# Kernel optimization log

Hardware: AMD Instinct MI355X
Metric: run time of the kernel (lower is better)

Reference implementation:

```python
import jax, jax.numpy as jnp
import numpy as np

B, T, D, H = 2, 2048, 1024, 16
HD = D // H            # 64
FH = 2752              # SwiGLU hidden: round64(int(2*4*D/3))
BETA_INIT = 0.5


def rmsnorm(x, w, eps=1e-6):
    x32 = x.astype(jnp.float32)
    r = jax.lax.rsqrt(jnp.mean(x32 * x32, axis=-1, keepdims=True) + eps)
    return (x32 * r).astype(x.dtype) * w


def rope(x, cos, sin):
    # x: (B,H,T,HD); cos/sin: (T,HD//2)
    d2 = x.shape[-1] // 2
    x1, x2 = x[..., :d2], x[..., d2:]
    return jnp.concatenate([x1 * cos - x2 * sin, x2 * cos + x1 * sin], axis=-1)


def delta_res(x, h, gn_w, g_w, g_b, wv_w, eps_k=1e-6):
    # k-hat = normalize(h); k = k_hat / sqrt(d)
    h32 = h.astype(jnp.float32)
    nrm = jnp.sqrt(jnp.sum(h32 * h32, axis=-1, keepdims=True))
    k = (h32 / jnp.maximum(nrm, eps_k)).astype(x.dtype) * (1.0 / np.sqrt(D))
    c = rmsnorm(x, gn_w)
    logit = c @ g_w + g_b                                   # (B,T)
    beta = (2.0 * jax.nn.sigmoid(logit.astype(jnp.float32))).astype(x.dtype)[..., None]
    v = jax.nn.sigmoid(x @ wv_w)[..., None]                 # (B,T,1)
    kTx = jnp.sum(k * x, axis=-1, keepdims=True)
    return x + beta * (v - kTx) * k


def setup_inputs() -> dict:
    key = jax.random.key(0)
    ks = jax.random.split(key, 12)
    s = 0.02
    gb = np.float32(np.log(BETA_INIT / 2.0 / (1.0 - BETA_INIT / 2.0 + 1e-8)))
    return {
        "x": jax.random.normal(ks[0], (B, T, D), jnp.float32),
        "wq": jax.random.normal(ks[1], (D, D), jnp.float32) * s,
        "wk": jax.random.normal(ks[2], (D, D), jnp.float32) * s,
        "wv": jax.random.normal(ks[3], (D, D), jnp.float32) * s,
        "wo": jax.random.normal(ks[4], (D, D), jnp.float32) * s,
        "qn_w": jnp.ones((HD,), jnp.float32),
        "kn_w": jnp.ones((HD,), jnp.float32),
        "attn_norm_w": jnp.ones((D,), jnp.float32),
        "g1_norm_w": jnp.ones((D,), jnp.float32),
        "g1_w": jax.random.normal(ks[5], (D,), jnp.float32) * s,
        "g1_b": jnp.asarray(gb),
        "wv1": jax.random.normal(ks[6], (D,), jnp.float32) * s,
        "mlp_norm_w": jnp.ones((D,), jnp.float32),
        "w1": jax.random.normal(ks[7], (FH, D), jnp.float32) * s,
        "w2": jax.random.normal(ks[8], (D, FH), jnp.float32) * s,
        "w3": jax.random.normal(ks[9], (FH, D), jnp.float32) * s,
        "g2_norm_w": jnp.ones((D,), jnp.float32),
        "g2_w": jax.random.normal(ks[10], (D,), jnp.float32) * s,
        "g2_b": jnp.asarray(gb),
        "wv2": jax.random.normal(ks[11], (D,), jnp.float32) * s,
    }


def reference(x, wq, wk, wv, wo, qn_w, kn_w, attn_norm_w,
              g1_norm_w, g1_w, g1_b, wv1, mlp_norm_w, w1, w2, w3,
              g2_norm_w, g2_w, g2_b, wv2):
    # ---- attention sublayer (pre-norm) ----
    xc = rmsnorm(x, attn_norm_w)
    q = (xc @ wq.T).reshape(B, T, H, HD).swapaxes(1, 2)   # (B,H,T,HD)
    k = (xc @ wk.T).reshape(B, T, H, HD).swapaxes(1, 2)
    v = (xc @ wv.T).reshape(B, T, H, HD).swapaxes(1, 2)
    q = rmsnorm(q, qn_w)
    k = rmsnorm(k, kn_w)
    inv_freq = 1.0 / (10000.0 ** (jnp.arange(0, HD, 2, dtype=jnp.float32) / HD))
    freqs = jnp.arange(T, dtype=jnp.float32)[:, None] * inv_freq[None, :]  # (T,HD/2)
    cos, sin = jnp.cos(freqs), jnp.sin(freqs)
    q = rope(q, cos, sin)
    k = rope(k, cos, sin)
    scale = 1.0 / np.sqrt(HD)
    scores = jnp.einsum('bhqd,bhkd->bhqk', q, k) * scale
    causal = jnp.where(jnp.arange(T)[:, None] >= jnp.arange(T)[None, :], 0.0, -jnp.inf).astype(scores.dtype)
    attn = jax.nn.softmax(scores + causal, axis=-1)
    out = jnp.einsum('bhqk,bhkd->bhqd', attn, v)
    h_attn = out.swapaxes(1, 2).reshape(B, T, D) @ wo.T
    x = delta_res(x, h_attn, g1_norm_w, g1_w, g1_b, wv1)
    # ---- MLP sublayer (pre-norm SwiGLU) ----
    xm = rmsnorm(x, mlp_norm_w)
    h_mlp = (jax.nn.silu(xm @ w1.T) * (xm @ w3.T)) @ w2.T
    x = delta_res(x, h_mlp, g2_norm_w, g2_w, g2_b, wv2)
    return x
```

## Files before the change

### kernel.cpp

```cpp
#include <hip/hip_runtime.h>
#include <hip/hip_bf16.h>
#include <math.h>

using bf16 = __hip_bfloat16;
typedef __bf16 bf16x8 __attribute__((ext_vector_type(8)));
typedef float f32x4 __attribute__((ext_vector_type(4)));

static constexpr int B_ = 2, T_ = 2048, D_ = 1024, H_ = 16, HD_ = 64, FH_ = 2752;
static constexpr int BT = B_ * T_;

struct __align__(8)  bh4 { bf16 h[4]; };
struct __align__(16) bh8 { bf16 h[8]; };

#define DEV static __device__ __forceinline__

DEV float b2f(bf16 v) { return __bfloat162float(v); }
DEV bf16  f2b(float v) { return __float2bfloat16(v); }
DEV __bf16 f2bb(float f) { __hip_bfloat16 h = __float2bfloat16(f); return *reinterpret_cast<__bf16*>(&h); }
DEV float sigmoidf_(float x) { return 1.0f / (1.0f + __expf(-x)); }

DEV void load4f(const bf16* p, float* v) {
    bh4 t = *reinterpret_cast<const bh4*>(p);
#pragma unroll
    for (int i = 0; i < 4; ++i) v[i] = b2f(t.h[i]);
}
DEV void load4f(const float* p, float* v) {
    float4 t = *reinterpret_cast<const float4*>(p);
    v[0] = t.x; v[1] = t.y; v[2] = t.z; v[3] = t.w;
}
DEV void store4(float* p, const float* v) {
    float4 t; t.x = v[0]; t.y = v[1]; t.z = v[2]; t.w = v[3];
    *reinterpret_cast<float4*>(p) = t;
}
DEV float waveReduceSum(float v) {
#pragma unroll
    for (int m = 32; m; m >>= 1) v += __shfl_xor(v, m);
    return v;
}

DEV void gl_lds16(const bf16* g, bf16* lds_base) {
    __builtin_amdgcn_global_load_lds(
        (const __attribute__((address_space(1))) void*)g,
        (__attribute__((address_space(3))) void*)lds_base, 16, 0, 0);
}

__global__ __launch_bounds__(256) void k_rope_tables(float* __restrict__ cost, float* __restrict__ sint) {
    int idx = blockIdx.x * 256 + threadIdx.x;
    if (idx >= T_ * 32) return;
    int t = idx >> 5, j = idx & 31;
    float inv = powf(10000.0f, -(float)j * (1.0f / 32.0f));
    float f = (float)t * inv;
    cost[idx] = cosf(f);
    sint[idx] = sinf(f);
}

__global__ __launch_bounds__(256) void k_f2b(const float* __restrict__ in, bf16* __restrict__ out, int n8) {
    int i = blockIdx.x * 256 + threadIdx.x;
    if (i >= n8) return;
    const float4* p = reinterpret_cast<const float4*>(in + (size_t)i * 8);
    float4 a = p[0], b = p[1];
    bh8 o;
    o.h[0] = f2b(a.x); o.h[1] = f2b(a.y); o.h[2] = f2b(a.z); o.h[3] = f2b(a.w);
    o.h[4] = f2b(b.x); o.h[5] = f2b(b.y); o.h[6] = f2b(b.z); o.h[7] = f2b(b.w);
    *reinterpret_cast<bh8*>(out + (size_t)i * 8) = o;
}

__global__ __launch_bounds__(256) void k_rmsnorm(const float* __restrict__ x, const float* __restrict__ w,
                                                 bf16* __restrict__ out) {
    int row = blockIdx.x, tid = threadIdx.x;
    const float* xr = x + (size_t)row * D_;
    int base = tid * 4;
    float v[4];
    load4f(xr + base, v);
    float ss = v[0]*v[0] + v[1]*v[1] + v[2]*v[2] + v[3]*v[3];
    ss = waveReduceSum(ss);
    __shared__ float red[4];
    if ((tid & 63) == 0) red[tid >> 6] = ss;
    __syncthreads();
    ss = red[0] + red[1] + red[2] + red[3];
    float r = rsqrtf(ss * (1.0f / D_) + 1e-6f);
    float wv[4];
    load4f(w + base, wv);
    bh4 o;
#pragma unroll
    for (int i = 0; i < 4; ++i) o.h[i] = f2b(v[i] * r * wv[i]);
    *reinterpret_cast<bh4*>(out + (size_t)row * D_ + base) = o;
}

template <bool GATE>
__global__ __launch_bounds__(256) void k_gemm_db(const bf16* __restrict__ A, const bf16* __restrict__ W,
                                                 bf16* __restrict__ C, int M, int N, int K) {
    __shared__ bf16 sA[2][128 * 32];
    __shared__ bf16 sB[2][128 * 32];
    int tid = threadIdx.x, lane = tid & 63, wid = tid >> 6;
    int m0 = blockIdx.x * 128, n0 = blockIdx.y * 128;
    int wr = wid >> 1, wc = wid & 1;
    int l16 = lane & 15, lg = lane >> 4;
    int srow = lane >> 2, scol = (lane & 3) * 8;

    f32x4 acc[4][4] = {};

#define STAGE(buf, k0)                                                                  \
    {                                                                                   \
        _Pragma("unroll")                                                               \
        for (int c = 0; c < 2; ++c) {                                                   \
            int r0 = wid * 32 + c * 16;                                                 \
            gl_lds16(&A[(size_t)(m0 + r0 + srow) * K + (k0) + scol], &sA[buf][r0 * 32]);\
        }                                                                               \
        _Pragma("unroll")                                                               \
        for (int c = 0; c < 2; ++c) {                                                   \
            int r0 = wid * 32 + c * 16;                                                 \
            int nrow = n0 + r0 + srow;                                                  \
            if (nrow > N - 1) nrow = N - 1;                                             \
            gl_lds16(&W[(size_t)nrow * K + (k0) + scol], &sB[buf][r0 * 32]);            \
        }                                                                               \
    }

    STAGE(0, 0);
    __syncthreads();
    int nk = K >> 5;
    int cur = 0;
    for (int t = 0; t < nk; ++t) {
        if (t + 1 < nk) STAGE(cur ^ 1, (t + 1) * 32);
        bf16x8 af[4], bfr[4];
#pragma unroll
        for (int m = 0; m < 4; ++m)
            af[m] = *reinterpret_cast<const bf16x8*>(&sA[cur][(wr * 64 + m * 16 + l16) * 32 + lg * 8]);
#pragma unroll
        for (int n = 0; n < 4; ++n)
            bfr[n] = *reinterpret_cast<const bf16x8*>(&sB[cur][(wc * 64 + n * 16 + l16) * 32 + lg * 8]);
#pragma unroll
        for (int m = 0; m < 4; ++m)
#pragma unroll
            for (int n = 0; n < 4; ++n)
                acc[m][n] = __builtin_amdgcn_mfma_f32_16x16x32_bf16(af[m], bfr[n], acc[m][n], 0, 0, 0);
        __syncthreads();
        cur ^= 1;
    }
#undef STAGE

    int rbase = m0 + wr * 64, cbase = n0 + wc * 64;
#pragma unroll
    for (int m = 0; m < 4; ++m) {
#pragma unroll
        for (int n = 0; n < 4; ++n) {
            int col = cbase + n * 16 + l16;
            if (col < N) {
#pragma unroll
                for (int r = 0; r < 4; ++r) {
                    int row = rbase + m * 16 + lg * 4 + r;
                    size_t idx = (size_t)row * N + col;
                    if (GATE) {
                        float g = b2f(C[idx]);
                        C[idx] = f2b(g * sigmoidf_(g) * acc[m][n][r]);
                    } else {
                        C[idx] = f2b(acc[m][n][r]);
                    }
                }
            }
        }
    }
}

__global__ __launch_bounds__(256) void k_qk_norm_rope(const bf16* __restrict__ qin, const float* __restrict__ wn,
                                                      const float* __restrict__ cost, const float* __restrict__ sint,
                                                      bf16* __restrict__ qout, float scale, int ld, int off) {
    int tid = threadIdx.x;
    int g = blockIdx.x * 4 + (tid >> 6);
    int d = tid & 63;
    int h = g % H_, t = (g / H_) % T_, b = g / (H_ * T_);
    float v = b2f(qin[(size_t)(b * T_ + t) * ld + off + h * HD_ + d]);
    float ss = waveReduceSum(v * v);
    float r = rsqrtf(ss * (1.0f / HD_) + 1e-6f);
    float xn = v * r * wn[d];
    float p = __shfl_xor(xn, 32);
    float c = cost[t * 32 + (d & 31)], s = sint[t * 32 + (d & 31)];
    float o = (d < 32) ? (xn * c - p * s) : (xn * c + p * s);
    qout[((size_t)(b * H_ + h) * T_ + t) * HD_ + d] = f2b(o * scale);
}

__global__ __launch_bounds__(256) void k_v_transpose(const bf16* __restrict__ vin, bf16* __restrict__ vt,
                                                     int ld, int off) {
    __shared__ bf16 tile[64][72];
    int tid = threadIdx.x;
    int bh = blockIdx.y;
    int t0 = blockIdx.x * 64;
    int b = bh >> 4, h = bh & 15;
#pragma unroll
    for (int i = 0; i < 16; ++i) {
        int lin = i * 256 + tid;
        int tl = lin >> 6, d = lin & 63;
        tile[tl][d] = vin[(size_t)(b * T_ + t0 + tl) * ld + off + h * HD_ + d];
    }
    __syncthreads();
#pragma unroll
    for (int i = 0; i < 16; ++i) {
        int lin = i * 256 + tid;
        int d = lin >> 6, tl = lin & 63;
        vt[((size_t)bh * HD_ + d) * T_ + t0 + tl] = tile[tl][d];
    }
}

template <bool MASKED>
DEV void fa3_tile(const bf16* __restrict__ kl, const bf16* __restrict__ vl,
                  int l16, int lg, int qloc,
                  const bf16x8 qf0, const bf16x8 qf1,
                  f32x4* acc, float& m_r, float& l_r) {
    f32x4 s[8];
#pragma unroll
    for (int n = 0; n < 8; ++n) {
        int kv = n * 16 + l16;
        bf16x8 kf0 = *reinterpret_cast<const bf16x8*>(&kl[kv * 64 + (((lg ^ kv) & 7) << 3)]);
        bf16x8 kf1 = *reinterpret_cast<const bf16x8*>(&kl[kv * 64 + ((((4 + lg) ^ kv) & 7) << 3)]);
        f32x4 t = {};
        t = __builtin_amdgcn_mfma_f32_16x16x32_bf16(kf0, qf0, t, 0, 0, 0);
        t = __builtin_amdgcn_mfma_f32_16x16x32_bf16(kf1, qf1, t, 0, 0, 0);
        s[n] = t;
    }
    if (MASKED) {
#pragma unroll
        for (int n = 0; n < 8; ++n)
#pragma unroll
            for (int r = 0; r < 4; ++r)
                if (n * 16 + lg * 4 + r > qloc) s[n][r] = -INFINITY;
    }
    float mx = -INFINITY;
#pragma unroll
    for (int n = 0; n < 8; ++n)
#pragma unroll
        for (int r = 0; r < 4; ++r) mx = fmaxf(mx, s[n][r]);
    mx = fmaxf(mx, __shfl_xor(mx, 16));
    mx = fmaxf(mx, __shfl_xor(mx, 32));
    float mnew = fmaxf(m_r, mx);
    float corr = __expf(m_r - mnew);
    m_r = mnew;
    float ps = 0.0f;
#pragma unroll
    for (int n = 0; n < 8; ++n)
#pragma unroll
        for (int r = 0; r < 4; ++r) {
            float e = __expf(s[n][r] - mnew);
            s[n][r] = e;
            ps += e;
        }
    l_r = l_r * corr + ps;
#pragma unroll
    for (int np = 0; np < 4; ++np) acc[np] = acc[np] * corr;

    bf16x8 pb[4];
#pragma unroll
    for (int n2 = 0; n2 < 4; ++n2)
#pragma unroll
        for (int j = 0; j < 8; ++j)
            pb[n2][j] = f2bb(s[2 * n2 + (j >> 2)][j & 3]);

    int d15 = l16;
    int eoff = (lg & 1) * 4;
#pragma unroll
    for (int n2 = 0; n2 < 4; ++n2) {
        int c0 = (n2 * 4 + (lg >> 1));
        int c1 = c0 + 2;
#pragma unroll
        for (int np = 0; np < 4; ++np) {
            int d = np * 16 + l16;
            union { bf16x8 v; bh4 q[2]; } u;
            u.q[0] = *reinterpret_cast<const bh4*>(&vl[d * 128 + ((c0 ^ d15) << 3) + eoff]);
            u.q[1] = *reinterpret_cast<const bh4*>(&vl[d * 128 + ((c1 ^ d15) << 3) + eoff]);
            acc[np] = __builtin_amdgcn_mfma_f32_16x16x32_bf16(u.v, pb[n2], acc[np], 0, 0, 0);
        }
    }
}

__global__ __launch_bounds__(256) void k_flash(const bf16* __restrict__ Q, const bf16* __restrict__ Kk,
                                               const bf16* __restrict__ Vt, bf16* __restrict__ Out) {
    __shared__ bf16 kl[128 * 64];
    __shared__ bf16 vl[64 * 128];
    int tid = threadIdx.x, lane = tid & 63, w = tid >> 6;
    int l16 = lane & 15, lg = lane >> 4;
    int L = blockIdx.x;
    int xcd = L & 7, m = L >> 3;
    int bh = xcd * 4 + (m & 3);
    int qi = (T_ / 128 - 1) - (m >> 2);
    int q0 = qi * 128;
    int b = bh >> 4, h = bh & 15;
    const bf16* qb = Q + (size_t)bh * T_ * HD_;
    const bf16* kb = Kk + (size_t)bh * T_ * HD_;
    const bf16* vb = Vt + (size_t)bh * HD_ * T_;

    bf16x8 qfr[2][2];
#pragma unroll
    for (int f = 0; f < 2; ++f) {
        int qrow = q0 + w * 32 + f * 16 + l16;
        const bf16* qp = qb + (size_t)qrow * HD_ + lg * 8;
        qfr[f][0] = *reinterpret_cast<const bf16x8*>(qp);
        qfr[f][1] = *reinterpret_cast<const bf16x8*>(qp + 32);
    }
    f32x4 acc[2][4] = {};
    float m_r[2] = {-INFINITY, -INFINITY};
    float l_r[2] = {0.0f, 0.0f};

    for (int kv0 = 0; kv0 <= q0; kv0 += 128) {
        __syncthreads();
#pragma unroll
        for (int i = 0; i < 4; ++i) {
            int idx = i * 256 + tid;
            int kv = idx >> 3, c = idx & 7;
            *reinterpret_cast<bh8*>(&kl[kv * 64 + (((c ^ kv) & 7) << 3)]) =
                *reinterpret_cast<const bh8*>(&kb[(size_t)(kv0 + kv) * HD_ + c * 8]);
        }
#pragma unroll
        for (int i = 0; i < 4; ++i) {
            int idx = i * 256 + tid;
            int d = idx >> 4, c = idx & 15;
            *reinterpret_cast<bh8*>(&vl[d * 128 + (((c ^ d) & 15) << 3)]) =
                *reinterpret_cast<const bh8*>(&vb[(size_t)d * T_ + kv0 + c * 8]);
        }
        __syncthreads();
        if (kv0 == q0) {
#pragma unroll
            for (int f = 0; f < 2; ++f)
                fa3_tile<true>(kl, vl, l16, lg, w * 32 + f * 16 + l16,
                               qfr[f][0], qfr[f][1], acc[f], m_r[f], l_r[f]);
        } else {
#pragma unroll
            for (int f = 0; f < 2; ++f)
                fa3_tile<false>(kl, vl, l16, lg, 0,
                                qfr[f][0], qfr[f][1], acc[f], m_r[f], l_r[f]);
        }
    }
#pragma unroll
    for (int f = 0; f < 2; ++f) {
        float lt = l_r[f];
        lt += __shfl_xor(lt, 16);
        lt += __shfl_xor(lt, 32);
        float inv = 1.0f / lt;
        int qrow = q0 + w * 32 + f * 16 + l16;
#pragma unroll
        for (int np = 0; np < 4; ++np) {
            bh4 o;
#pragma unroll
            for (int r = 0; r < 4; ++r) o.h[r] = f2b(acc[f][np][r] * inv);
            *reinterpret_cast<bh4*>(&Out[(size_t)(b * T_ + qrow) * D_ + h * HD_ + np * 16 + lg * 4]) = o;
        }
    }
}

template <typename TIN, typename TOUT>
__global__ __launch_bounds__(256) void k_delta_res(const TIN* __restrict__ x, const bf16* __restrict__ h,
                                                   const float* __restrict__ gn_w, const float* __restrict__ g_w,
                                                   const float* __restrict__ g_b, const float* __restrict__ wv_w,
                                                   TOUT* __restrict__ out) {
    int row = blockIdx.x, tid = threadIdx.x;
    int base = tid * 4;
    float xv[4], hv[4], gnv[4], gwv[4], wvv[4];
    load4f(x + (size_t)row * D_ + base, xv);
    load4f(h + (size_t)row * D_ + base, hv);
    load4f(gn_w + base, gnv);
    load4f(g_w + base, gwv);
    load4f(wv_w + base, wvv);
    float s_h2 = 0, s_x2 = 0, s_xg = 0, s_xv = 0, s_hx = 0;
#pragma unroll
    for (int i = 0; i < 4; ++i) {
        s_h2 += hv[i] * hv[i];
        s_x2 += xv[i] * xv[i];
        s_xg += xv[i] * gnv[i] * gwv[i];
        s_xv += xv[i] * wvv[i];
        s_hx += hv[i] * xv[i];
    }
    s_h2 = waveReduceSum(s_h2); s_x2 = waveReduceSum(s_x2); s_xg = waveReduceSum(s_xg);
    s_xv = waveReduceSum(s_xv); s_hx = waveReduceSum(s_hx);
    __shared__ float red[4][5];
    int wid = tid >> 6;
    if ((tid & 63) == 0) {
        red[wid][0] = s_h2; red[wid][1] = s_x2; red[wid][2] = s_xg;
        red[wid][3] = s_xv; red[wid][4] = s_hx;
    }
    __syncthreads();
    s_h2 = red[0][0] + red[1][0] + red[2][0] + red[3][0];
    s_x2 = red[0][1] + red[1][1] + red[2][1] + red[3][1];
    s_xg = red[0][2] + red[1][2] + red[2][2] + red[3][2];
    s_xv = red[0][3] + red[1][3] + red[2][3] + red[3][3];
    s_hx = red[0][4] + red[1][4] + red[2][4] + red[3][4];

    float r = rsqrtf(s_x2 * (1.0f / D_) + 1e-6f);
    float logit = r * s_xg + g_b[0];
    float beta = 2.0f * sigmoidf_(logit);
    float vsig = sigmoidf_(s_xv);
    float nrm = sqrtf(s_h2);
    float ks = (1.0f / 32.0f) / fmaxf(nrm, 1e-6f);
    float coef = beta * (vsig - ks * s_hx) * ks;
    float o[4];
#pragma unroll
    for (int i = 0; i < 4; ++i) o[i] = xv[i] + coef * hv[i];
    store4(out + (size_t)row * D_ + base, o);
}

extern "C" void kernel_launch(void* const* d_in, const int* in_sizes, int n_in,
                              void* d_out, int out_size, void* d_ws, size_t ws_size,
                              hipStream_t stream) {
    const float* x       = (const float*)d_in[0];
    const float* wq      = (const float*)d_in[1];
    const float* wk      = (const float*)d_in[2];
    const float* wv      = (const float*)d_in[3];
    const float* wo      = (const float*)d_in[4];
    const float* qn_w    = (const float*)d_in[5];
    const float* kn_w    = (const float*)d_in[6];
    const float* attn_nw = (const float*)d_in[7];
    const float* g1_nw   = (const float*)d_in[8];
    const float* g1_w    = (const float*)d_in[9];
    const float* g1_b    = (const float*)d_in[10];
    const float* wv1     = (const float*)d_in[11];
    const float* mlp_nw  = (const float*)d_in[12];
    const float* w1      = (const float*)d_in[13];
    const float* w2      = (const float*)d_in[14];
    const float* w3      = (const float*)d_in[15];
    const float* g2_nw   = (const float*)d_in[16];
    const float* g2_w    = (const float*)d_in[17];
    const float* g2_b    = (const float*)d_in[18];
    const float* wv2     = (const float*)d_in[19];
    float* out = (float*)d_out;

    char* ws = (char*)d_ws;
    const size_t KB = 1024;
    const size_t MB = 1024 * 1024;
    float* cost = (float*)(ws);
    float* sint = (float*)(ws + 256 * KB);
    bf16* XC = (bf16*)(ws + 512 * KB);
    bf16* Bb = (bf16*)(ws + 512 * KB + 8  * MB);
    bf16* Cb = (bf16*)(ws + 512 * KB + 16 * MB);
    bf16* Db = (bf16*)(ws + 512 * KB + 24 * MB);
    bf16* Eb = (bf16*)(ws + 512 * KB + 32 * MB);
    bf16* Fb = (bf16*)(ws + 512 * KB + 40 * MB);
    bf16* Gb = (bf16*)(ws + 512 * KB + 48 * MB);
    float* x1 = (float*)(ws + 512 * KB + 56 * MB);

    bf16* wqkv = Eb;
    bf16* qkv  = Bb;
    bf16* wbo  = XC;
    bf16* attn_out = Bb;
    bf16* wffn = Bb;
    bf16* h1   = Eb;
    bf16* hmlp = XC;

    const int nDD = D_ * D_ / 8, nFD = FH_ * D_ / 8;
    dim3 blk(256);

    k_rope_tables<<<dim3((T_ * 32) / 256), blk, 0, stream>>>(cost, sint);

    k_rmsnorm<<<dim3(BT), blk, 0, stream>>>(x, attn_nw, XC);
    k_f2b<<<dim3((nDD + 255) / 256), blk, 0, stream>>>(wq, wqkv, nDD);
    k_f2b<<<dim3((nDD + 255) / 256), blk, 0, stream>>>(wk, wqkv + (size_t)D_ * D_, nDD);
    k_f2b<<<dim3((nDD + 255) / 256), blk, 0, stream>>>(wv, wqkv + (size_t)2 * D_ * D_, nDD);

    dim3 gqkv(BT / 128, 3 * D_ / 128);
    k_gemm_db<false><<<gqkv, blk, 0, stream>>>(XC, wqkv, qkv, BT, 3 * D_, D_);

    k_qk_norm_rope<<<dim3(BT * H_ / 4), blk, 0, stream>>>(qkv, qn_w, cost, sint, Eb, 0.125f, 3 * D_, 0);
    k_qk_norm_rope<<<dim3(BT * H_ / 4), blk, 0, stream>>>(qkv, kn_w, cost, sint, Fb, 1.0f, 3 * D_, D_);
    k_v_transpose<<<dim3(T_ / 64, B_ * H_), blk, 0, stream>>>(qkv, Gb, 3 * D_, 2 * D_);

    k_f2b<<<dim3((nDD + 255) / 256), blk, 0, stream>>>(wo, wbo, nDD);
    k_flash<<<dim3((T_ / 128) * B_ * H_), blk, 0, stream>>>(Eb, Fb, Gb, attn_out);

    dim3 gdd(BT / 128, D_ / 128);
    k_gemm_db<false><<<gdd, blk, 0, stream>>>(attn_out, wbo, Cb, BT, D_, D_);

    k_delta_res<float, float><<<dim3(BT), blk, 0, stream>>>(x, Cb, g1_nw, g1_w, g1_b, wv1, x1);
    k_rmsnorm<<<dim3(BT), blk, 0, stream>>>(x1, mlp_nw, XC);

    dim3 gffn(BT / 128, (FH_ + 127) / 128);
    k_f2b<<<dim3((nFD + 255) / 256), blk, 0, stream>>>(w1, wffn, nFD);
    k_gemm_db<false><<<gffn, blk, 0, stream>>>(XC, wffn, h1, BT, FH_, D_);
    k_f2b<<<dim3((nFD + 255) / 256), blk, 0, stream>>>(w3, wffn, nFD);
    k_gemm_db<true><<<gffn, blk, 0, stream>>>(XC, wffn, h1, BT, FH_, D_);
    k_f2b<<<dim3((nFD + 255) / 256), blk, 0, stream>>>(w2, wffn, nFD);
    k_gemm_db<false><<<gdd, blk, 0, stream>>>(h1, wffn, hmlp, BT, D_, FH_);

    k_delta_res<float, float><<<dim3(BT), blk, 0, stream>>>(x1, hmlp, g2_nw, g2_w, g2_b, wv2, out);
}
```

Before: 327.8 us.

## Fuse w1/w3 GEMMs via interleaved weights, swizzle LDS, narrow N tiles

Interleaves w1 and w3 rows in blocks of 16 during bf16 conversion, so a single GEMM computes both projections and applies SiLU gating in the epilogue. This removes one GEMM launch, the re-read of XC, and the h1 round-trip through memory. It also XOR-swizzles the LDS column chunks to reduce bank conflicts. The N=1024 GEMMs switch to 64-wide N tiles so the wo and w2 projections launch more blocks. The risk is the extra cost of the interleaving kernel and the lower per-wave MFMA reuse in the BN=64 path.

After: 284.7 us. 13.2% less time.

```diff
diff --git a/kernel.cpp b/kernel.cpp
--- a/kernel.cpp
+++ b/kernel.cpp
@@ -63,6 +63,22 @@
     o.h[0] = f2b(a.x); o.h[1] = f2b(a.y); o.h[2] = f2b(a.z); o.h[3] = f2b(a.w);
     o.h[4] = f2b(b.x); o.h[5] = f2b(b.y); o.h[6] = f2b(b.z); o.h[7] = f2b(b.w);
     *reinterpret_cast<bh8*>(out + (size_t)i * 8) = o;
+}
+
+__global__ __launch_bounds__(256) void k_f2b_pair(const float* __restrict__ w1, const float* __restrict__ w3,
+                                                  bf16* __restrict__ outp, int n8tot) {
+    int i = blockIdx.x * 256 + threadIdx.x;
+    if (i >= n8tot) return;
+    int r = i >> 7, c8 = i & 127;
+    int sel = (r >> 4) & 1;
+    int j = ((r >> 5) << 4) | (r & 15);
+    const float* src = (sel ? w3 : w1) + (size_t)j * D_ + c8 * 8;
+    float4 a = reinterpret_cast<const float4*>(src)[0];
+    float4 b = reinterpret_cast<const float4*>(src)[1];
+    bh8 o;
+    o.h[0] = f2b(a.x); o.h[1] = f2b(a.y); o.h[2] = f2b(a.z); o.h[3] = f2b(a.w);
+    o.h[4] = f2b(b.x); o.h[5] = f2b(b.y); o.h[6] = f2b(b.z); o.h[7] = f2b(b.w);
+    *reinterpret_cast<bh8*>(outp + (size_t)r * D_ + c8 * 8) = o;
 }
 
 __global__ __launch_bounds__(256) void k_rmsnorm(const float* __restrict__ x, const float* __restrict__ w,
@@ -87,18 +103,23 @@
     *reinterpret_cast<bh4*>(out + (size_t)row * D_ + base) = o;
 }
 
-template <bool GATE>
+template <int BN, int EPI>
 __global__ __launch_bounds__(256) void k_gemm_db(const bf16* __restrict__ A, const bf16* __restrict__ W,
                                                  bf16* __restrict__ C, int M, int N, int K) {
+    constexpr int MR = (BN == 128) ? 4 : 2;
+    constexpr int WR = (BN == 128) ? 64 : 32;
     __shared__ bf16 sA[2][128 * 32];
-    __shared__ bf16 sB[2][128 * 32];
+    __shared__ bf16 sB[2][BN * 32];
     int tid = threadIdx.x, lane = tid & 63, wid = tid >> 6;
-    int m0 = blockIdx.x * 128, n0 = blockIdx.y * 128;
-    int wr = wid >> 1, wc = wid & 1;
+    int m0 = blockIdx.x * 128, n0 = blockIdx.y * BN;
+    int wr, wc;
+    if (BN == 128) { wr = wid >> 1; wc = wid & 1; } else { wr = wid; wc = 0; }
     int l16 = lane & 15, lg = lane >> 4;
-    int srow = lane >> 2, scol = (lane & 3) * 8;
-
-    f32x4 acc[4][4] = {};
+    int srow = lane >> 2;
+    int scol = ((lane & 3) ^ (srow & 3)) * 8;
+    int rchunk = (lg ^ (l16 & 3)) * 8;
+
+    f32x4 acc[MR][4] = {};
 
 #define STAGE(buf, k0)                                                                  \
     {                                                                                   \
@@ -107,9 +128,16 @@
             int r0 = wid * 32 + c * 16;                                                 \
             gl_lds16(&A[(size_t)(m0 + r0 + srow) * K + (k0) + scol], &sA[buf][r0 * 32]);\
         }                                                                               \
-        _Pragma("unroll")                                                               \
-        for (int c = 0; c < 2; ++c) {                                                   \
-            int r0 = wid * 32 + c * 16;                                                 \
+        if (BN == 128) {                                                                \
+            _Pragma("unroll")                                                           \
+            for (int c = 0; c < 2; ++c) {                                               \
+                int r0 = wid * 32 + c * 16;                                             \
+                int nrow = n0 + r0 + srow;                                              \
+                if (nrow > N - 1) nrow = N - 1;                                         \
+                gl_lds16(&W[(size_t)nrow * K + (k0) + scol], &sB[buf][r0 * 32]);        \
+            }                                                                           \
+        } else {                                                                        \
+            int r0 = wid * 16;                                                          \
             int nrow = n0 + r0 + srow;                                                  \
             if (nrow > N - 1) nrow = N - 1;                                             \
             gl_lds16(&W[(size_t)nrow * K + (k0) + scol], &sB[buf][r0 * 32]);            \
@@ -122,15 +150,15 @@
     int cur = 0;
     for (int t = 0; t < nk; ++t) {
         if (t + 1 < nk) STAGE(cur ^ 1, (t + 1) * 32);
-        bf16x8 af[4], bfr[4];
-#pragma unroll
-        for (int m = 0; m < 4; ++m)
-            af[m] = *reinterpret_cast<const bf16x8*>(&sA[cur][(wr * 64 + m * 16 + l16) * 32 + lg * 8]);
+        bf16x8 af[MR], bfr[4];
+#pragma unroll
+        for (int m = 0; m < MR; ++m)
+            af[m] = *reinterpret_cast<const bf16x8*>(&sA[cur][(wr * WR + m * 16 + l16) * 32 + rchunk]);
 #pragma unroll
         for (int n = 0; n < 4; ++n)
-            bfr[n] = *reinterpret_cast<const bf16x8*>(&sB[cur][(wc * 64 + n * 16 + l16) * 32 + lg * 8]);
-#pragma unroll
-        for (int m = 0; m < 4; ++m)
+            bfr[n] = *reinterpret_cast<const bf16x8*>(&sB[cur][(wc * 64 + n * 16 + l16) * 32 + rchunk]);
+#pragma unroll
+        for (int m = 0; m < MR; ++m)
 #pragma unroll
             for (int n = 0; n < 4; ++n)
                 acc[m][n] = __builtin_amdgcn_mfma_f32_16x16x32_bf16(af[m], bfr[n], acc[m][n], 0, 0, 0);
@@ -139,22 +167,35 @@
     }
 #undef STAGE
 
-    int rbase = m0 + wr * 64, cbase = n0 + wc * 64;
-#pragma unroll
-    for (int m = 0; m < 4; ++m) {
-#pragma unroll
-        for (int n = 0; n < 4; ++n) {
-            int col = cbase + n * 16 + l16;
-            if (col < N) {
+    int rbase = m0 + wr * WR, cbase = n0 + wc * 64;
+    if (EPI == 1) {
+        int Ng = N >> 1;
+        int gbase = (n0 >> 1) + wc * 32;
+#pragma unroll
+        for (int m = 0; m < MR; ++m) {
+#pragma unroll
+            for (int n2 = 0; n2 < 2; ++n2) {
+                int gcol = gbase + n2 * 16 + l16;
 #pragma unroll
                 for (int r = 0; r < 4; ++r) {
                     int row = rbase + m * 16 + lg * 4 + r;
-                    size_t idx = (size_t)row * N + col;
-                    if (GATE) {
-                        float g = b2f(C[idx]);
-                        C[idx] = f2b(g * sigmoidf_(g) * acc[m][n][r]);
-                    } else {
-                        C[idx] = f2b(acc[m][n][r]);
+                    float a1 = acc[m][n2 * 2][r];
+                    float a3 = acc[m][n2 * 2 + 1][r];
+                    C[(size_t)row * Ng + gcol] = f2b(a1 * sigmoidf_(a1) * a3);
+                }
+            }
+        }
+    } else {
+#pragma unroll
+        for (int m = 0; m < MR; ++m) {
+#pragma unroll
+            for (int n = 0; n < 4; ++n) {
+                int col = cbase + n * 16 + l16;
+                if (col < N) {
+#pragma unroll
+                    for (int r = 0; r < 4; ++r) {
+                        int row = rbase + m * 16 + lg * 4 + r;
+                        C[(size_t)row * N + col] = f2b(acc[m][n][r]);
                     }
                 }
             }
@@ -438,8 +479,9 @@
     bf16* qkv  = Bb;
     bf16* wbo  = XC;
     bf16* attn_out = Bb;
-    bf16* wffn = Bb;
-    bf16* h1   = Eb;
+    bf16* wpair = Bb;
+    bf16* w2b  = Db;
+    bf16* g    = Eb;
     bf16* hmlp = XC;
 
     const int nDD = D_ * D_ / 8, nFD = FH_ * D_ / 8;
@@ -453,7 +495,7 @@
     k_f2b<<<dim3((nDD + 255) / 256), blk, 0, stream>>>(wv, wqkv + (size_t)2 * D_ * D_, nDD);
 
     dim3 gqkv(BT / 128, 3 * D_ / 128);
-    k_gemm_db<false><<<gqkv, blk, 0, stream>>>(XC, wqkv, qkv, BT, 3 * D_, D_);
+    k_gemm_db<128, 0><<<gqkv, blk, 0, stream>>>(XC, wqkv, qkv, BT, 3 * D_, D_);
 
     k_qk_norm_rope<<<dim3(BT * H_ / 4), blk, 0, stream>>>(qkv, qn_w, cost, sint, Eb, 0.125f, 3 * D_, 0);
     k_qk_norm_rope<<<dim3(BT * H_ / 4), blk, 0, stream>>>(qkv, kn_w, cost, sint, Fb, 1.0f, 3 * D_, D_);
@@ -462,19 +504,21 @@
     k_f2b<<<dim3((nDD + 255) / 256), blk, 0, stream>>>(wo, wbo, nDD);
     k_flash<<<dim3((T_ / 128) * B_ * H_), blk, 0, stream>>>(Eb, Fb, Gb, attn_out);
 
-    dim3 gdd(BT / 128, D_ / 128);
-    k_gemm_db<false><<<gdd, blk, 0, stream>>>(attn_out, wbo, Cb, BT, D_, D_);
+    dim3 gwo(BT / 128, D_ / 64);
+    k_gemm_db<64, 0><<<gwo, blk, 0, stream>>>(attn_out, wbo, Cb, BT, D_, D_);
 
     k_delta_res<float, float><<<dim3(BT), blk, 0, stream>>>(x, Cb, g1_nw, g1_w, g1_b, wv1, x1);
+
+    k_f2b_pair<<<dim3((2 * nFD + 255) / 256), blk, 0, stream>>>(w1, w3, wpair, 2 * nFD);
+    k_f2b<<<dim3((nFD + 255) / 256), blk, 0, stream>>>(w2, w2b, nFD);
+
     k_rmsnorm<<<dim3(BT), blk, 0, stream>>>(x1, mlp_nw, XC);
 
-    dim3 gffn(BT / 128, (FH_ + 127) / 128);
-    k_f2b<<<dim3((nFD + 255) / 256), blk, 0, stream>>>(w1, wffn, nFD);
-    k_gemm_db<false><<<gffn, blk, 0, stream>>>(XC, wffn, h1, BT, FH_, D_);
-    k_f2b<<<dim3((nFD + 255) / 256), blk, 0, stream>>>(w3, wffn, nFD);
-    k_gemm_db<true><<<gffn, blk, 0, stream>>>(XC, wffn, h1, BT, FH_, D_);
-    k_f2b<<<dim3((nFD + 255) / 256), blk, 0, stream>>>(w2, wffn, nFD);
-    k_gemm_db<false><<<gdd, blk, 0, stream>>>(h1, wffn, hmlp, BT, D_, FH_);
+    dim3 gffn(BT / 128, (2 * FH_) / 128);
+    k_gemm_db<128, 1><<<gffn, blk, 0, stream>>>(XC, wpair, g, BT, 2 * FH_, D_);
+
+    dim3 gw2(BT / 128, D_ / 64);
+    k_gemm_db<64, 0><<<gw2, blk, 0, stream>>>(g, w2b, hmlp, BT, D_, FH_);
 
     k_delta_res<float, float><<<dim3(BT), blk, 0, stream>>>(x1, hmlp, g2_nw, g2_w, g2_b, wv2, out);
 }
```
